# Kernel tuning notes

Measured on AMD Instinct MI355X. Metric: run time of the kernel, lower is better.

The kernel has to match this reference:

```python
import jax, jax.numpy as jnp
import numpy as np

NUM_AGENTS = 256
HIDDEN = 1024
RANK = 32
LOG_ALPHA_INIT = -1.0
ALPHA_MAX = 5.0
LN_EPS = 1e-5


def setup_inputs() -> dict:
    key = jax.random.key(0)
    k_h, k_ids, k_u, k_v = jax.random.split(key, 4)
    scale = 1.0 / (RANK ** 0.5)
    h = jax.random.normal(k_h, (8192, HIDDEN), dtype=jnp.float32)
    agent_ids = jax.random.randint(k_ids, (8192,), 0, NUM_AGENTS)
    # per-agent fixed random projections (buffers in the original module)
    projection_u = jax.random.normal(k_u, (NUM_AGENTS, HIDDEN, RANK), dtype=jnp.float32) * scale
    projection_v = jax.random.normal(k_v, (NUM_AGENTS, RANK, HIDDEN), dtype=jnp.float32) * scale
    log_alpha = jnp.asarray(LOG_ALPHA_INIT, dtype=jnp.float32)
    ln_gamma = jnp.ones((HIDDEN,), dtype=jnp.float32)
    ln_beta = jnp.zeros((HIDDEN,), dtype=jnp.float32)
    return {
        "h": h,
        "log_alpha": log_alpha,
        "ln_gamma": ln_gamma,
        "ln_beta": ln_beta,
        "projection_u": projection_u,
        "projection_v": projection_v,
        "agent_ids": agent_ids,
    }


def reference(h, log_alpha, ln_gamma, ln_beta, projection_u, projection_v, agent_ids):
    ids = agent_ids % NUM_AGENTS  # [B]
    u = projection_u[ids]  # [B, H, R] gathered per token
    v = projection_v[ids]  # [B, R, H]
    intermediate = jnp.einsum('bh,bhr->br', h, u)      # [B, R]
    perturbation = jnp.einsum('br,brh->bh', intermediate, v)  # [B, H]
    alpha = jnp.minimum(jnp.exp(log_alpha), ALPHA_MAX)
    h_div = h + alpha * perturbation
    # LayerNorm over last dim (biased variance, eps=1e-5)
    mean = jnp.mean(h_div, axis=-1, keepdims=True)
    var = jnp.mean(jnp.square(h_div - mean), axis=-1, keepdims=True)
    h_div = (h_div - mean) * jax.lax.rsqrt(var + LN_EPS) * ln_gamma + ln_beta
    return h_div
```

## Files before the change

kernel.cpp:

```cpp
#include <hip/hip_runtime.h>
#include <math.h>

#define NUM_AGENTS 256
#define HIDDEN 1024
#define RANK 32
#define NTOK 8192
#define TBATCH 8
#define LISTCAP 64
#define NSLOT 4
#define ALPHA_MAX 5.0f
#define LN_EPS 1e-5f

typedef float f32x4 __attribute__((ext_vector_type(4)));

__global__ __launch_bounds__(256) void scan_kernel(
    const int* __restrict__ ids, int* __restrict__ counts, int* __restrict__ lists)
{
    __shared__ int toklist[LISTCAP];
    __shared__ int cnt;
    const int t = threadIdx.x;
    const int agent = blockIdx.x;
    if (t == 0) { cnt = 0; toklist[0] = 0; }
    __syncthreads();
    #pragma unroll
    for (int it = 0; it < NTOK / 1024; ++it) {
        int4 v = ((const int4*)ids)[t + 256 * it];
        int ib = 4 * (t + 256 * it);
        if ((v.x & (NUM_AGENTS - 1)) == agent) { int p = atomicAdd(&cnt, 1); if (p < LISTCAP) toklist[p] = ib + 0; }
        if ((v.y & (NUM_AGENTS - 1)) == agent) { int p = atomicAdd(&cnt, 1); if (p < LISTCAP) toklist[p] = ib + 1; }
        if ((v.z & (NUM_AGENTS - 1)) == agent) { int p = atomicAdd(&cnt, 1); if (p < LISTCAP) toklist[p] = ib + 2; }
        if ((v.w & (NUM_AGENTS - 1)) == agent) { int p = atomicAdd(&cnt, 1); if (p < LISTCAP) toklist[p] = ib + 3; }
    }
    __syncthreads();
    const int c = min(cnt, LISTCAP);
    if (t == 0) counts[agent] = c;
    if (t < LISTCAP)
        lists[agent * LISTCAP + t] = toklist[min(t, max(c - 1, 0))];
}

__global__ __launch_bounds__(256) void div_inject_kernel(
    const float* __restrict__ hglob,
    const float* __restrict__ log_alpha,
    const float* __restrict__ gamma,
    const float* __restrict__ beta,
    const float* __restrict__ U,
    const float* __restrict__ V,
    const int* __restrict__ counts,
    const int* __restrict__ lists,
    float* __restrict__ out)
{
    __shared__ __align__(16) float Hs[TBATCH][HIDDEN];
    float* red0  = &Hs[0][0];
    float* inter = red0;
    float* wred  = red0 + 256;

    const int t = threadIdx.x;
    const int x = blockIdx.x & 7;
    const int rest = blockIdx.x >> 3;
    const int s = rest & 3;
    const int jc = rest >> 2;
    const int a = x + 8 * jc;

    const int cnt = counts[a];
    const int ng = (cnt + TBATCH - 1) / TBATCH;
    if (s >= ng) return;

    const float* Ua = U + (size_t)a * (HIDDEN * RANK);
    const float* Va = V + (size_t)a * (RANK * HIDDEN);

    const int r4 = (t & 7) * 4;
    const int ks = t >> 3;
    const int c  = t * 4;
    const int wave = t >> 6, lane = t & 63;

    const float alpha = fminf(__expf(log_alpha[0]), ALPHA_MAX);
    const float4 gv = *(const float4*)(gamma + c);
    const float4 bv = *(const float4*)(beta + c);

    for (int g = s; g < ng; g += NSLOT) {
        const int nm = min(TBATCH, cnt - g * TBATCH);

        const int* gl = lists + a * LISTCAP + g * TBATCH;
        int tk[TBATCH];
        #pragma unroll
        for (int m = 0; m < TBATCH; ++m) tk[m] = gl[m];

        float4 ub[2][4];
        #pragma unroll
        for (int j = 0; j < 4; ++j)
            ub[0][j] = *(const float4*)(Ua + (ks + 32 * j) * RANK + r4);

        f32x4 h0v;
        {
            f32x4 hv[TBATCH];
            #pragma unroll
            for (int m = 0; m < TBATCH; ++m)
                hv[m] = __builtin_nontemporal_load((const f32x4*)(hglob + (size_t)tk[m] * HIDDEN + c));
            h0v = hv[0];
            #pragma unroll
            for (int m = 0; m < TBATCH; ++m)
                *(f32x4*)(&Hs[m][c]) = hv[m];
        }
        __syncthreads();

        float4 acc[TBATCH];
        #pragma unroll
        for (int m = 0; m < TBATCH; ++m) acc[m] = make_float4(0.f, 0.f, 0.f, 0.f);
        #pragma unroll
        for (int jb = 0; jb < 8; ++jb) {
            const int cur = jb & 1;
            if (jb < 7) {
                #pragma unroll
                for (int j = 0; j < 4; ++j)
                    ub[cur ^ 1][j] = *(const float4*)(Ua + (ks + 32 * (4 * (jb + 1) + j)) * RANK + r4);
            }
            #pragma unroll
            for (int j = 0; j < 4; ++j) {
                const int hh = ks + 32 * (4 * jb + j);
                float4 u = ub[cur][j];
                #pragma unroll
                for (int m = 0; m < TBATCH; ++m) {
                    float h0 = Hs[m][hh];
                    acc[m].x += h0 * u.x;
                    acc[m].y += h0 * u.y;
                    acc[m].z += h0 * u.z;
                    acc[m].w += h0 * u.w;
                }
            }
        }
        #pragma unroll
        for (int off = 8; off <= 32; off <<= 1) {
            #pragma unroll
            for (int m = 0; m < TBATCH; ++m) {
                acc[m].x += __shfl_xor(acc[m].x, off, 64);
                acc[m].y += __shfl_xor(acc[m].y, off, 64);
                acc[m].z += __shfl_xor(acc[m].z, off, 64);
                acc[m].w += __shfl_xor(acc[m].w, off, 64);
            }
        }
        __syncthreads();
        if (lane < 8) {
            #pragma unroll
            for (int m = 0; m < TBATCH; ++m)
                *(float4*)(&red0[wave * 256 + m * 32 + r4]) = acc[m];
        }

        float4 vb[2][4];
        #pragma unroll
        for (int j = 0; j < 4; ++j)
            vb[0][j] = *(const float4*)(Va + j * HIDDEN + c);

        __syncthreads();
        {
            int m = t >> 5, rr = t & 31;
            inter[m * 32 + rr] = red0[m * 32 + rr] + red0[256 + m * 32 + rr]
                               + red0[512 + m * 32 + rr] + red0[768 + m * 32 + rr];
        }
        __syncthreads();

        float4 p[TBATCH];
        #pragma unroll
        for (int m = 0; m < TBATCH; ++m) p[m] = make_float4(0.f, 0.f, 0.f, 0.f);
        #pragma unroll
        for (int rb = 0; rb < 8; ++rb) {
            const int cur = rb & 1;
            if (rb < 7) {
                #pragma unroll
                for (int j = 0; j < 4; ++j)
                    vb[cur ^ 1][j] = *(const float4*)(Va + (4 * (rb + 1) + j) * HIDDEN + c);
            }
            #pragma unroll
            for (int j = 0; j < 4; ++j) {
                const int r = 4 * rb + j;
                float4 v = vb[cur][j];
                #pragma unroll
                for (int m = 0; m < TBATCH; ++m) {
                    float ir = inter[m * 32 + r];
                    p[m].x += ir * v.x;
                    p[m].y += ir * v.y;
                    p[m].z += ir * v.z;
                    p[m].w += ir * v.w;
                }
            }
        }

        float sred[TBATCH], q[TBATCH];
        #pragma unroll
        for (int m = 0; m < TBATCH; ++m) {
            f32x4 h4 = (m == 0) ? h0v : *(const f32x4*)(&Hs[m][c]);
            p[m].x = h4.x + alpha * p[m].x;
            p[m].y = h4.y + alpha * p[m].y;
            p[m].z = h4.z + alpha * p[m].z;
            p[m].w = h4.w + alpha * p[m].w;
            sred[m] = p[m].x + p[m].y + p[m].z + p[m].w;
            q[m] = p[m].x * p[m].x + p[m].y * p[m].y + p[m].z * p[m].z + p[m].w * p[m].w;
        }
        #pragma unroll
        for (int off = 32; off > 0; off >>= 1) {
            #pragma unroll
            for (int m = 0; m < TBATCH; ++m) {
                sred[m] += __shfl_xor(sred[m], off, 64);
                q[m] += __shfl_xor(q[m], off, 64);
            }
        }
        if (lane == 0) {
            #pragma unroll
            for (int m = 0; m < TBATCH; ++m) {
                wred[wave * 16 + m] = sred[m];
                wred[wave * 16 + 8 + m] = q[m];
            }
        }
        __syncthreads();

        #pragma unroll
        for (int m = 0; m < TBATCH; ++m) {
            if (m < nm) {
                float S = wred[m] + wred[16 + m] + wred[32 + m] + wred[48 + m];
                float Q = wred[8 + m] + wred[24 + m] + wred[40 + m] + wred[56 + m];
                float mean = S * (1.0f / HIDDEN);
                float rstd = rsqrtf(Q * (1.0f / HIDDEN) - mean * mean + LN_EPS);
                f32x4 o;
                o.x = (p[m].x - mean) * rstd * gv.x + bv.x;
                o.y = (p[m].y - mean) * rstd * gv.y + bv.y;
                o.z = (p[m].z - mean) * rstd * gv.z + bv.z;
                o.w = (p[m].w - mean) * rstd * gv.w + bv.w;
                __builtin_nontemporal_store(o, (f32x4*)(out + (size_t)tk[m] * HIDDEN + c));
            }
        }
        if (g + NSLOT < ng) __syncthreads();
    }
}

extern "C" void kernel_launch(void* const* d_in, const int* in_sizes, int n_in,
                              void* d_out, int out_size, void* d_ws, size_t ws_size,
                              hipStream_t stream) {
    const float* h     = (const float*)d_in[0];
    const float* la    = (const float*)d_in[1];
    const float* gamma = (const float*)d_in[2];
    const float* beta  = (const float*)d_in[3];
    const float* U     = (const float*)d_in[4];
    const float* V     = (const float*)d_in[5];
    const int* ids     = (const int*)d_in[6];
    float* out         = (float*)d_out;

    int* counts = (int*)d_ws;
    int* lists  = counts + NUM_AGENTS;

    scan_kernel<<<NUM_AGENTS, 256, 0, stream>>>(ids, counts, lists);
    div_inject_kernel<<<NUM_AGENTS * NSLOT, 256, 0, stream>>>(
        h, la, gamma, beta, U, V, counts, lists, out);
}
```

Baseline: 201.3 us.

## Use 512-thread blocks handling 16 tokens per agent with shared U/V reuse

Each block now has two 256-thread halves, each processing 8 tokens of the same agent, so one block covers 16 tokens. This replaces the old 8-token-per-slot loop. The two halves read identical U and V rows, so those weights can be served from L1, and the number of blocks streaming each agent's projections roughly halves. In exchange, LDS per block doubles to 64KB, which may cut resident blocks per CU. The agent-to-block index mapping also changes and drops the previous interleaving.

```diff
diff --git a/kernel.cpp b/kernel.cpp
--- a/kernel.cpp
+++ b/kernel.cpp
@@ -5,7 +5,8 @@
 #define HIDDEN 1024
 #define RANK 32
 #define NTOK 8192
-#define TBATCH 8
+#define TBATCH 16
+#define HB 8
 #define LISTCAP 64
 #define NSLOT 4
 #define ALPHA_MAX 5.0f
@@ -38,7 +39,7 @@
         lists[agent * LISTCAP + t] = toklist[min(t, max(c - 1, 0))];
 }
 
-__global__ __launch_bounds__(256) void div_inject_kernel(
+__global__ __launch_bounds__(512) void div_inject_kernel(
     const float* __restrict__ hglob,
     const float* __restrict__ log_alpha,
     const float* __restrict__ gamma,
@@ -50,184 +51,177 @@
     float* __restrict__ out)
 {
     __shared__ __align__(16) float Hs[TBATCH][HIDDEN];
-    float* red0  = &Hs[0][0];
-    float* inter = red0;
-    float* wred  = red0 + 256;
 
     const int t = threadIdx.x;
-    const int x = blockIdx.x & 7;
-    const int rest = blockIdx.x >> 3;
-    const int s = rest & 3;
-    const int jc = rest >> 2;
-    const int a = x + 8 * jc;
+    const int a = blockIdx.x & (NUM_AGENTS - 1);
+    const int slot = blockIdx.x >> 8;
 
     const int cnt = counts[a];
-    const int ng = (cnt + TBATCH - 1) / TBATCH;
-    if (s >= ng) return;
+    if (slot * TBATCH >= cnt) return;
+    const int nm = min(TBATCH, cnt - slot * TBATCH);
+
+    const int th = t & 255;
+    const int mbase = (t >> 8) * HB;
+    const int nmh = min(max(nm - mbase, 0), HB);
+
+    float* red0h = &Hs[mbase][0];
+    float* interh = red0h;
+    float* wredh = red0h + 256;
 
     const float* Ua = U + (size_t)a * (HIDDEN * RANK);
     const float* Va = V + (size_t)a * (RANK * HIDDEN);
 
-    const int r4 = (t & 7) * 4;
-    const int ks = t >> 3;
-    const int c  = t * 4;
-    const int wave = t >> 6, lane = t & 63;
+    const int r4 = (th & 7) * 4;
+    const int ks = th >> 3;
+    const int c  = th * 4;
+    const int wave = th >> 6, lane = t & 63;
+
+    float4 ub[2][4];
+    #pragma unroll
+    for (int j = 0; j < 4; ++j)
+        ub[0][j] = *(const float4*)(Ua + (ks + 32 * j) * RANK + r4);
+
+    const int* gl = lists + a * LISTCAP + slot * TBATCH + mbase;
+    int tk[HB];
+    #pragma unroll
+    for (int m = 0; m < HB; ++m) tk[m] = __builtin_amdgcn_readfirstlane(gl[m]);
 
     const float alpha = fminf(__expf(log_alpha[0]), ALPHA_MAX);
+
+    f32x4 h0v;
+    {
+        f32x4 hv[HB];
+        #pragma unroll
+        for (int m = 0; m < HB; ++m)
+            hv[m] = __builtin_nontemporal_load((const f32x4*)(hglob + (size_t)tk[m] * HIDDEN + c));
+        h0v = hv[0];
+        #pragma unroll
+        for (int m = 0; m < HB; ++m)
+            *(f32x4*)(&Hs[mbase + m][c]) = hv[m];
+    }
+    __syncthreads();
+
+    float4 acc[HB];
+    #pragma unroll
+    for (int m = 0; m < HB; ++m) acc[m] = make_float4(0.f, 0.f, 0.f, 0.f);
+    #pragma unroll
+    for (int jb = 0; jb < 8; ++jb) {
+        const int cur = jb & 1;
+        if (jb < 7) {
+            #pragma unroll
+            for (int j = 0; j < 4; ++j)
+                ub[cur ^ 1][j] = *(const float4*)(Ua + (ks + 32 * (4 * (jb + 1) + j)) * RANK + r4);
+        }
+        #pragma unroll
+        for (int j = 0; j < 4; ++j) {
+            const int hh = ks + 32 * (4 * jb + j);
+            float4 u = ub[cur][j];
+            #pragma unroll
+            for (int m = 0; m < HB; ++m) {
+                float h0 = Hs[mbase + m][hh];
+                acc[m].x += h0 * u.x;
+                acc[m].y += h0 * u.y;
+                acc[m].z += h0 * u.z;
+                acc[m].w += h0 * u.w;
+            }
+        }
+    }
+    #pragma unroll
+    for (int off = 8; off <= 32; off <<= 1) {
+        #pragma unroll
+        for (int m = 0; m < HB; ++m) {
+            acc[m].x += __shfl_xor(acc[m].x, off, 64);
+            acc[m].y += __shfl_xor(acc[m].y, off, 64);
+            acc[m].z += __shfl_xor(acc[m].z, off, 64);
+            acc[m].w += __shfl_xor(acc[m].w, off, 64);
+        }
+    }
+    __syncthreads();
+    if (lane < 8) {
+        #pragma unroll
+        for (int m = 0; m < HB; ++m)
+            *(float4*)(&red0h[wave * 256 + m * 32 + r4]) = acc[m];
+    }
+
+    float4 vb[2][4];
+    #pragma unroll
+    for (int j = 0; j < 4; ++j)
+        vb[0][j] = *(const float4*)(Va + j * HIDDEN + c);
+
+    __syncthreads();
+    interh[th] = red0h[th] + red0h[256 + th] + red0h[512 + th] + red0h[768 + th];
+    __syncthreads();
+
+    float4 p[HB];
+    #pragma unroll
+    for (int m = 0; m < HB; ++m) p[m] = make_float4(0.f, 0.f, 0.f, 0.f);
+    #pragma unroll
+    for (int rb = 0; rb < 8; ++rb) {
+        const int cur = rb & 1;
+        if (rb < 7) {
+            #pragma unroll
+            for (int j = 0; j < 4; ++j)
+                vb[cur ^ 1][j] = *(const float4*)(Va + (4 * (rb + 1) + j) * HIDDEN + c);
+        }
+        #pragma unroll
+        for (int j = 0; j < 4; ++j) {
+            const int r = 4 * rb + j;
+            float4 v = vb[cur][j];
+            #pragma unroll
+            for (int m = 0; m < HB; ++m) {
+                float ir = interh[m * 32 + r];
+                p[m].x += ir * v.x;
+                p[m].y += ir * v.y;
+                p[m].z += ir * v.z;
+                p[m].w += ir * v.w;
+            }
+        }
+    }
+
+    float sred[HB], q[HB];
+    #pragma unroll
+    for (int m = 0; m < HB; ++m) {
+        f32x4 h4 = (m == 0) ? h0v : *(const f32x4*)(&Hs[mbase + m][c]);
+        p[m].x = h4.x + alpha * p[m].x;
+        p[m].y = h4.y + alpha * p[m].y;
+        p[m].z = h4.z + alpha * p[m].z;
+        p[m].w = h4.w + alpha * p[m].w;
+        sred[m] = p[m].x + p[m].y + p[m].z + p[m].w;
+        q[m] = p[m].x * p[m].x + p[m].y * p[m].y + p[m].z * p[m].z + p[m].w * p[m].w;
+    }
+    #pragma unroll
+    for (int off = 32; off > 0; off >>= 1) {
+        #pragma unroll
+        for (int m = 0; m < HB; ++m) {
+            sred[m] += __shfl_xor(sred[m], off, 64);
+            q[m] += __shfl_xor(q[m], off, 64);
+        }
+    }
+    if (lane == 0) {
+        #pragma unroll
+        for (int m = 0; m < HB; ++m) {
+            wredh[wave * 16 + m] = sred[m];
+            wredh[wave * 16 + 8 + m] = q[m];
+        }
+    }
+    __syncthreads();
+
     const float4 gv = *(const float4*)(gamma + c);
     const float4 bv = *(const float4*)(beta + c);
-
-    for (int g = s; g < ng; g += NSLOT) {
-        const int nm = min(TBATCH, cnt - g * TBATCH);
-
-        const int* gl = lists + a * LISTCAP + g * TBATCH;
-        int tk[TBATCH];
-        #pragma unroll
-        for (int m = 0; m < TBATCH; ++m) tk[m] = gl[m];
-
-        float4 ub[2][4];
-        #pragma unroll
-        for (int j = 0; j < 4; ++j)
-            ub[0][j] = *(const float4*)(Ua + (ks + 32 * j) * RANK + r4);
-
-        f32x4 h0v;
-        {
-            f32x4 hv[TBATCH];
-            #pragma unroll
-            for (int m = 0; m < TBATCH; ++m)
-                hv[m] = __builtin_nontemporal_load((const f32x4*)(hglob + (size_t)tk[m] * HIDDEN + c));
-            h0v = hv[0];
-            #pragma unroll
-            for (int m = 0; m < TBATCH; ++m)
-                *(f32x4*)(&Hs[m][c]) = hv[m];
-        }
-        __syncthreads();
-
-        float4 acc[TBATCH];
-        #pragma unroll
-        for (int m = 0; m < TBATCH; ++m) acc[m] = make_float4(0.f, 0.f, 0.f, 0.f);
-        #pragma unroll
-        for (int jb = 0; jb < 8; ++jb) {
-            const int cur = jb & 1;
-            if (jb < 7) {
-                #pragma unroll
-                for (int j = 0; j < 4; ++j)
-                    ub[cur ^ 1][j] = *(const float4*)(Ua + (ks + 32 * (4 * (jb + 1) + j)) * RANK + r4);
-            }
-            #pragma unroll
-            for (int j = 0; j < 4; ++j) {
-                const int hh = ks + 32 * (4 * jb + j);
-                float4 u = ub[cur][j];
-                #pragma unroll
-                for (int m = 0; m < TBATCH; ++m) {
-                    float h0 = Hs[m][hh];
-                    acc[m].x += h0 * u.x;
-                    acc[m].y += h0 * u.y;
-                    acc[m].z += h0 * u.z;
-                    acc[m].w += h0 * u.w;
-                }
-            }
-        }
-        #pragma unroll
-        for (int off = 8; off <= 32; off <<= 1) {
-            #pragma unroll
-            for (int m = 0; m < TBATCH; ++m) {
-                acc[m].x += __shfl_xor(acc[m].x, off, 64);
-                acc[m].y += __shfl_xor(acc[m].y, off, 64);
-                acc[m].z += __shfl_xor(acc[m].z, off, 64);
-                acc[m].w += __shfl_xor(acc[m].w, off, 64);
-            }
-        }
-        __syncthreads();
-        if (lane < 8) {
-            #pragma unroll
-            for (int m = 0; m < TBATCH; ++m)
-                *(float4*)(&red0[wave * 256 + m * 32 + r4]) = acc[m];
-        }
-
-        float4 vb[2][4];
-        #pragma unroll
-        for (int j = 0; j < 4; ++j)
-            vb[0][j] = *(const float4*)(Va + j * HIDDEN + c);
-
-        __syncthreads();
-        {
-            int m = t >> 5, rr = t & 31;
-            inter[m * 32 + rr] = red0[m * 32 + rr] + red0[256 + m * 32 + rr]
-                               + red0[512 + m * 32 + rr] + red0[768 + m * 32 + rr];
-        }
-        __syncthreads();
-
-        float4 p[TBATCH];
-        #pragma unroll
-        for (int m = 0; m < TBATCH; ++m) p[m] = make_float4(0.f, 0.f, 0.f, 0.f);
-        #pragma unroll
-        for (int rb = 0; rb < 8; ++rb) {
-            const int cur = rb & 1;
-            if (rb < 7) {
-                #pragma unroll
-                for (int j = 0; j < 4; ++j)
-                    vb[cur ^ 1][j] = *(const float4*)(Va + (4 * (rb + 1) + j) * HIDDEN + c);
-            }
-            #pragma unroll
-            for (int j = 0; j < 4; ++j) {
-                const int r = 4 * rb + j;
-                float4 v = vb[cur][j];
-                #pragma unroll
-                for (int m = 0; m < TBATCH; ++m) {
-                    float ir = inter[m * 32 + r];
-                    p[m].x += ir * v.x;
-                    p[m].y += ir * v.y;
-                    p[m].z += ir * v.z;
-                    p[m].w += ir * v.w;
-                }
-            }
-        }
-
-        float sred[TBATCH], q[TBATCH];
-        #pragma unroll
-        for (int m = 0; m < TBATCH; ++m) {
-            f32x4 h4 = (m == 0) ? h0v : *(const f32x4*)(&Hs[m][c]);
-            p[m].x = h4.x + alpha * p[m].x;
-            p[m].y = h4.y + alpha * p[m].y;
-            p[m].z = h4.z + alpha * p[m].z;
-            p[m].w = h4.w + alpha * p[m].w;
-            sred[m] = p[m].x + p[m].y + p[m].z + p[m].w;
-            q[m] = p[m].x * p[m].x + p[m].y * p[m].y + p[m].z * p[m].z + p[m].w * p[m].w;
-        }
-        #pragma unroll
-        for (int off = 32; off > 0; off >>= 1) {
-            #pragma unroll
-            for (int m = 0; m < TBATCH; ++m) {
-                sred[m] += __shfl_xor(sred[m], off, 64);
-                q[m] += __shfl_xor(q[m], off, 64);
-            }
-        }
-        if (lane == 0) {
-            #pragma unroll
-            for (int m = 0; m < TBATCH; ++m) {
-                wred[wave * 16 + m] = sred[m];
-                wred[wave * 16 + 8 + m] = q[m];
-            }
-        }
-        __syncthreads();
-
-        #pragma unroll
-        for (int m = 0; m < TBATCH; ++m) {
-            if (m < nm) {
-                float S = wred[m] + wred[16 + m] + wred[32 + m] + wred[48 + m];
-                float Q = wred[8 + m] + wred[24 + m] + wred[40 + m] + wred[56 + m];
-                float mean = S * (1.0f / HIDDEN);
-                float rstd = rsqrtf(Q * (1.0f / HIDDEN) - mean * mean + LN_EPS);
-                f32x4 o;
-                o.x = (p[m].x - mean) * rstd * gv.x + bv.x;
-                o.y = (p[m].y - mean) * rstd * gv.y + bv.y;
-                o.z = (p[m].z - mean) * rstd * gv.z + bv.z;
-                o.w = (p[m].w - mean) * rstd * gv.w + bv.w;
-                __builtin_nontemporal_store(o, (f32x4*)(out + (size_t)tk[m] * HIDDEN + c));
-            }
-        }
-        if (g + NSLOT < ng) __syncthreads();
+    #pragma unroll
+    for (int m = 0; m < HB; ++m) {
+        if (m < nmh) {
+            float S = wredh[m] + wredh[16 + m] + wredh[32 + m] + wredh[48 + m];
+            float Q = wredh[8 + m] + wredh[24 + m] + wredh[40 + m] + wredh[56 + m];
+            float mean = S * (1.0f / HIDDEN);
+            float rstd = rsqrtf(Q * (1.0f / HIDDEN) - mean * mean + LN_EPS);
+            f32x4 o;
+            o.x = (p[m].x - mean) * rstd * gv.x + bv.x;
+            o.y = (p[m].y - mean) * rstd * gv.y + bv.y;
+            o.z = (p[m].z - mean) * rstd * gv.z + bv.z;
+            o.w = (p[m].w - mean) * rstd * gv.w + bv.w;
+            __builtin_nontemporal_store(o, (f32x4*)(out + (size_t)tk[m] * HIDDEN + c));
+        }
     }
 }
 
@@ -247,6 +241,6 @@
     int* lists  = counts + NUM_AGENTS;
 
     scan_kernel<<<NUM_AGENTS, 256, 0, stream>>>(ids, counts, lists);
-    div_inject_kernel<<<NUM_AGENTS * NSLOT, 256, 0, stream>>>(
+    div_inject_kernel<<<NSLOT * NUM_AGENTS, 512, 0, stream>>>(
         h, la, gamma, beta, U, V, counts, lists, out);
 }
```

Measured after the change: 177.3 us. 11.9% less time.
